# Kernel tuning notes

Hardware: AMD Instinct MI355X
Metric: run time of the kernel (lower is better)

## Reference

```python
import jax, jax.numpy as jnp
import numpy as np

N_NODES = 50000
N_EDGES = 800000
D_IN = 256
D_OUT = 96


def setup_inputs() -> dict:
    key = jax.random.key(0)
    k1, k2, k3 = jax.random.split(key, 3)
    x = jax.random.normal(k1, (N_NODES, D_IN), dtype=jnp.float32)
    edge_index = jax.random.randint(k2, (2, N_EDGES), 0, N_NODES, dtype=jnp.int64)
    # Glorot-like init for the GCN weight, zeros bias (bias_init=zeros_)
    W = jax.random.normal(k3, (D_IN, D_OUT), dtype=jnp.float32) * (1.0 / np.sqrt(D_IN))
    b = jnp.zeros((D_OUT,), dtype=jnp.float32)
    return {"x": x, "edge_index": edge_index, "W": W, "b": b}


def reference(x, edge_index, W, b):
    # GCNConv with normalize=False, add_self_loops=False:
    #   h = x @ W                      [N, D_OUT]
    #   out[dst] = sum over edges of h[src]
    #   out += bias (added after aggregation)
    src, dst = edge_index[0], edge_index[1]
    h = x @ W                                  # dense projection [N, D_OUT]
    msgs = h[src]                              # gather [E, D_OUT]
    out = jax.ops.segment_sum(msgs, dst, num_segments=x.shape[0])  # scatter-add
    return out + b
```

## Files before the change

### kernel.cpp

```cpp
#include <hip/hip_runtime.h>
#include <hip/hip_bf16.h>

#define N_NODES 50000
#define N_EDGES 800000
#define D_IN 256
#define D_OUT 96

#define NB 196
#define CAP 5120
#define KA_EPT 16
#define KA_BLOCKS ((N_EDGES + 256 * KA_EPT - 1) / (256 * KA_EPT))

typedef short bf16x8 __attribute__((ext_vector_type(8)));
typedef float f32x4 __attribute__((ext_vector_type(4)));

static __device__ inline ushort f2bf(float f) {
    union { __hip_bfloat16 h; ushort s; } u;
    u.h = __float2bfloat16(f);
    return u.s;
}
static __device__ inline float bfhi2f(unsigned int hibits) {
    union { unsigned int u; float f; } v; v.u = hibits; return v.f;
}

__global__ __launch_bounds__(256) void gcn_wt_kernel(
    const float* __restrict__ W, ushort* __restrict__ wT) {
    int c = blockIdx.x;
    int k = threadIdx.x;
    wT[c * D_IN + k] = f2bf(W[k * D_OUT + c]);
}

#define WLDS_K 264

__global__ __launch_bounds__(256) void gcn_gemm_mfma(
    const float* __restrict__ x, const ushort* __restrict__ wT,
    ushort* __restrict__ hB) {
    __shared__ ushort Wlds[96 * WLDS_K];

    const int tid = threadIdx.x;
#pragma unroll
    for (int it = 0; it < 12; ++it) {
        int i   = tid + it * 256;
        int c   = i >> 5;
        int k8  = (i & 31) << 3;
        uint4 v = reinterpret_cast<const uint4*>(wT)[i];
        *reinterpret_cast<uint4*>(&Wlds[c * WLDS_K + k8]) = v;
    }
    __syncthreads();

    const int lane = tid & 63;
    const int wave = tid >> 6;
    const int l15  = lane & 15;
    const int lk   = (lane >> 4) * 8;
    const int arow = blockIdx.x * 64 + wave * 16 + l15;
    const bool aok = arow < N_NODES;
    const float* xrow = &x[(size_t)(aok ? arow : 0) * D_IN];

    f32x4 acc[6];
#pragma unroll
    for (int c = 0; c < 6; ++c) acc[c] = (f32x4){0.f, 0.f, 0.f, 0.f};

#pragma unroll
    for (int kc = 0; kc < D_IN; kc += 32) {
        float4 v0 = make_float4(0.f, 0.f, 0.f, 0.f);
        float4 v1 = make_float4(0.f, 0.f, 0.f, 0.f);
        if (aok) {
            v0 = *reinterpret_cast<const float4*>(&xrow[kc + lk]);
            v1 = *reinterpret_cast<const float4*>(&xrow[kc + lk + 4]);
        }
        bf16x8 a;
        a[0] = (short)f2bf(v0.x); a[1] = (short)f2bf(v0.y);
        a[2] = (short)f2bf(v0.z); a[3] = (short)f2bf(v0.w);
        a[4] = (short)f2bf(v1.x); a[5] = (short)f2bf(v1.y);
        a[6] = (short)f2bf(v1.z); a[7] = (short)f2bf(v1.w);
#pragma unroll
        for (int c = 0; c < 6; ++c) {
            bf16x8 bf = *reinterpret_cast<const bf16x8*>(
                &Wlds[(c * 16 + l15) * WLDS_K + kc + lk]);
            acc[c] = __builtin_amdgcn_mfma_f32_16x16x32_bf16(a, bf, acc[c], 0, 0, 0);
        }
    }

    const int rbase = blockIdx.x * 64 + wave * 16 + (lane >> 4) * 4;
#pragma unroll
    for (int r = 0; r < 4; ++r) {
        int orow = rbase + r;
        if (orow < N_NODES) {
#pragma unroll
            for (int c = 0; c < 6; ++c)
                hB[orow * D_OUT + c * 16 + l15] = f2bf(acc[c][r]);
        }
    }
}

__global__ __launch_bounds__(256) void gcn_partition_kernel(
    const int* __restrict__ ei, int* __restrict__ bucket_cursor,
    unsigned int* __restrict__ recs) {
    __shared__ int lhist[NB];
    __shared__ int lbase[NB];
    const int tid = threadIdx.x;
    if (tid < NB) lhist[tid] = 0;
    __syncthreads();

    const int e0 = blockIdx.x * (256 * KA_EPT) + tid;
    int bk[KA_EPT];
    int rk[KA_EPT];
    unsigned int rec[KA_EPT];
#pragma unroll
    for (int i = 0; i < KA_EPT; ++i) {
        int e = e0 + i * 256;
        bk[i] = -1;
        if (e < N_EDGES) {
            int src = ei[e];
            int dst = ei[N_EDGES + e];
            if ((unsigned)src < (unsigned)N_NODES && (unsigned)dst < (unsigned)N_NODES) {
                bk[i]  = dst >> 8;
                rec[i] = (unsigned)src | ((unsigned)(dst & 255) << 16);
                rk[i]  = atomicAdd(&lhist[bk[i]], 1);
            }
        }
    }
    __syncthreads();
    if (tid < NB) lbase[tid] = atomicAdd(&bucket_cursor[tid], lhist[tid]);
    __syncthreads();
#pragma unroll
    for (int i = 0; i < KA_EPT; ++i) {
        if (bk[i] >= 0) {
            int pos = lbase[bk[i]] + rk[i];
            if (pos < CAP)
                recs[bk[i] * CAP + pos] = rec[i];
        }
    }
}

__global__ __launch_bounds__(256) void gcn_bucket_csr_kernel(
    const unsigned int* __restrict__ recs, const int* __restrict__ bucket_cursor,
    ushort* __restrict__ sorted16, int* __restrict__ cnt, int* __restrict__ offs) {
    __shared__ int    hist[256];
    __shared__ int    scanb[256];
    __shared__ int    cur[256];
    __shared__ ushort loc[CAP];
    const int b = blockIdx.x;
    const int t = threadIdx.x;
    int size = bucket_cursor[b];
    if (size > CAP) size = CAP;

    hist[t] = 0;
    __syncthreads();
    for (int i = t; i < size; i += 256)
        atomicAdd(&hist[(recs[b * CAP + i] >> 16) & 255], 1);
    __syncthreads();

    int v = hist[t];
    scanb[t] = v;
    __syncthreads();
    for (int off = 1; off < 256; off <<= 1) {
        int u = (t >= off) ? scanb[t - off] : 0;
        __syncthreads();
        scanb[t] += u;
        __syncthreads();
    }
    int excl = scanb[t] - v;
    cur[t] = excl;
    __syncthreads();

    for (int i = t; i < size; i += 256) {
        unsigned int r = recs[b * CAP + i];
        int l = (r >> 16) & 255;
        int p = atomicAdd(&cur[l], 1);
        loc[p] = (ushort)(r & 0xffffu);
    }
    __syncthreads();

    for (int i = t; i < size; i += 256)
        sorted16[b * CAP + i] = loc[i];

    int node = b * 256 + t;
    if (node < N_NODES) {
        cnt[node]  = hist[t];
        offs[node] = b * CAP + excl;
    }
}

#define AGG_NPB 32

__global__ __launch_bounds__(384) void gcn_aggregate_kernel(
    const ushort* __restrict__ hB, const int* __restrict__ offs,
    const int* __restrict__ cnt, const ushort* __restrict__ sorted16,
    const float* __restrict__ b, float* __restrict__ out) {
    int t    = threadIdx.x;
    int nloc = t / 12;
    int d8   = t - nloc * 12;
    int node = blockIdx.x * AGG_NPB + nloc;
    if (node >= N_NODES) return;

    int start = offs[node];
    int deg   = cnt[node];

    float a[8];
#pragma unroll
    for (int j = 0; j < 8; ++j) a[j] = 0.f;

#define ACC8(v)                                           \
    a[0] += bfhi2f((v).x << 16);                          \
    a[1] += bfhi2f((v).x & 0xffff0000u);                  \
    a[2] += bfhi2f((v).y << 16);                          \
    a[3] += bfhi2f((v).y & 0xffff0000u);                  \
    a[4] += bfhi2f((v).z << 16);                          \
    a[5] += bfhi2f((v).z & 0xffff0000u);                  \
    a[6] += bfhi2f((v).w << 16);                          \
    a[7] += bfhi2f((v).w & 0xffff0000u);

    int i = 0;
    for (; i + 4 <= deg; i += 4) {
        int s0 = sorted16[start + i + 0];
        int s1 = sorted16[start + i + 1];
        int s2 = sorted16[start + i + 2];
        int s3 = sorted16[start + i + 3];
        uint4 v0 = *reinterpret_cast<const uint4*>(&hB[s0 * D_OUT + d8 * 8]);
        uint4 v1 = *reinterpret_cast<const uint4*>(&hB[s1 * D_OUT + d8 * 8]);
        uint4 v2 = *reinterpret_cast<const uint4*>(&hB[s2 * D_OUT + d8 * 8]);
        uint4 v3 = *reinterpret_cast<const uint4*>(&hB[s3 * D_OUT + d8 * 8]);
        ACC8(v0); ACC8(v1); ACC8(v2); ACC8(v3);
    }
    for (; i < deg; ++i) {
        int s = sorted16[start + i];
        uint4 v = *reinterpret_cast<const uint4*>(&hB[s * D_OUT + d8 * 8]);
        ACC8(v);
    }
#undef ACC8

    const float4* bp = reinterpret_cast<const float4*>(&b[d8 * 8]);
    float4 b0 = bp[0], b1 = bp[1];
    float4 o0 = make_float4(a[0] + b0.x, a[1] + b0.y, a[2] + b0.z, a[3] + b0.w);
    float4 o1 = make_float4(a[4] + b1.x, a[5] + b1.y, a[6] + b1.z, a[7] + b1.w);
    float4* op = reinterpret_cast<float4*>(&out[node * D_OUT + d8 * 8]);
    op[0] = o0;
    op[1] = o1;
}

extern "C" void kernel_launch(void* const* d_in, const int* in_sizes, int n_in,
                              void* d_out, int out_size, void* d_ws, size_t ws_size,
                              hipStream_t stream) {
    const float* x  = (const float*)d_in[0];
    const int*   ei = (const int*)d_in[1];
    const float* W  = (const float*)d_in[2];
    const float* b  = (const float*)d_in[3];
    float* out = (float*)d_out;

    char* ws = (char*)d_ws;
    ushort* hB            = (ushort*)(ws);
    ushort* wT            = (ushort*)(ws + 9600000);
    int*    cnt           = (int*)   (ws + 9649152);
    int*    offs          = (int*)   (ws + 9849152);
    int*    bucket_cursor = (int*)   (ws + 10049152);
    unsigned int* recs    = (unsigned int*)(ws + 10050176);
    ushort* sorted16      = (ushort*)(ws + 14064256);

    gcn_wt_kernel<<<dim3(96), 256, 0, stream>>>(W, wT);
    gcn_gemm_mfma<<<dim3((N_NODES + 63) / 64), 256, 0, stream>>>(x, wT, hB);

    hipMemsetAsync(bucket_cursor, 0, NB * sizeof(int), stream);
    gcn_partition_kernel<<<dim3(KA_BLOCKS), 256, 0, stream>>>(ei, bucket_cursor, recs);
    gcn_bucket_csr_kernel<<<dim3(NB), 256, 0, stream>>>(recs, bucket_cursor, sorted16, cnt, offs);

    gcn_aggregate_kernel<<<dim3((N_NODES + AGG_NPB - 1) / AGG_NPB), 384, 0, stream>>>(
        hB, offs, cnt, sorted16, b, out);
}
```

Measured before the change: 154.8 us.

## Fuse bucket CSR build with aggregation and fold cursor memset into weight kernel

Merges the per-bucket counting-sort kernel and the aggregation kernel into one kernel that sorts the source indices in LDS and then gathers straight from that LDS list. This removes the global sorted-index, count and offset arrays and one launch. Buckets shrink to 128 nodes (391 buckets, capacity 2560), and the hipMemsetAsync is replaced by zeroing the cursors inside the weight-transpose kernel. Each thread now accumulates 24 features instead of 8, which raises register pressure. Only 391 blocks run the aggregation, so there may be less parallelism to hide gather latency.

```diff
diff --git a/kernel.cpp b/kernel.cpp
--- a/kernel.cpp
+++ b/kernel.cpp
@@ -6,10 +6,12 @@
 #define D_IN 256
 #define D_OUT 96
 
-#define NB 196
-#define CAP 5120
-#define KA_EPT 16
-#define KA_BLOCKS ((N_EDGES + 256 * KA_EPT - 1) / (256 * KA_EPT))
+#define NBLK 391
+#define NTHR 512
+#define CAP  2560
+#define EPB  ((N_EDGES + NBLK - 1) / NBLK)
+#define EPT  ((EPB + NTHR - 1) / NTHR)
+#define WLDS_K 264
 
 typedef short bf16x8 __attribute__((ext_vector_type(8)));
 typedef float f32x4 __attribute__((ext_vector_type(4)));
@@ -24,13 +26,14 @@
 }
 
 __global__ __launch_bounds__(256) void gcn_wt_kernel(
-    const float* __restrict__ W, ushort* __restrict__ wT) {
+    const float* __restrict__ W, ushort* __restrict__ wT,
+    int* __restrict__ bucket_cursor) {
     int c = blockIdx.x;
     int k = threadIdx.x;
     wT[c * D_IN + k] = f2bf(W[k * D_OUT + c]);
-}
-
-#define WLDS_K 264
+    int gid = c * 256 + k;
+    if (gid < NBLK) bucket_cursor[gid] = 0;
+}
 
 __global__ __launch_bounds__(256) void gcn_gemm_mfma(
     const float* __restrict__ x, const ushort* __restrict__ wT,
@@ -93,38 +96,39 @@
     }
 }
 
-__global__ __launch_bounds__(256) void gcn_partition_kernel(
+__global__ __launch_bounds__(NTHR) void gcn_partition_kernel(
     const int* __restrict__ ei, int* __restrict__ bucket_cursor,
     unsigned int* __restrict__ recs) {
-    __shared__ int lhist[NB];
-    __shared__ int lbase[NB];
-    const int tid = threadIdx.x;
-    if (tid < NB) lhist[tid] = 0;
-    __syncthreads();
-
-    const int e0 = blockIdx.x * (256 * KA_EPT) + tid;
-    int bk[KA_EPT];
-    int rk[KA_EPT];
-    unsigned int rec[KA_EPT];
-#pragma unroll
-    for (int i = 0; i < KA_EPT; ++i) {
-        int e = e0 + i * 256;
+    __shared__ int lhist[NBLK];
+    __shared__ int lbase[NBLK];
+    const int t = threadIdx.x;
+    for (int i = t; i < NBLK; i += NTHR) lhist[i] = 0;
+    __syncthreads();
+
+    const int ebase = blockIdx.x * EPB;
+    const int eend  = min(ebase + EPB, N_EDGES);
+    int bk[EPT]; int rk[EPT]; unsigned int rec[EPT];
+#pragma unroll
+    for (int i = 0; i < EPT; ++i) {
+        int e = ebase + i * NTHR + t;
         bk[i] = -1;
-        if (e < N_EDGES) {
+        if (e < eend) {
             int src = ei[e];
             int dst = ei[N_EDGES + e];
-            if ((unsigned)src < (unsigned)N_NODES && (unsigned)dst < (unsigned)N_NODES) {
-                bk[i]  = dst >> 8;
-                rec[i] = (unsigned)src | ((unsigned)(dst & 255) << 16);
+            if ((unsigned)src < (unsigned)N_NODES &&
+                (unsigned)dst < (unsigned)N_NODES) {
+                bk[i]  = dst >> 7;
+                rec[i] = (unsigned)src | ((unsigned)(dst & 127) << 16);
                 rk[i]  = atomicAdd(&lhist[bk[i]], 1);
             }
         }
     }
     __syncthreads();
-    if (tid < NB) lbase[tid] = atomicAdd(&bucket_cursor[tid], lhist[tid]);
-    __syncthreads();
-#pragma unroll
-    for (int i = 0; i < KA_EPT; ++i) {
+    for (int i = t; i < NBLK; i += NTHR)
+        lbase[i] = atomicAdd(&bucket_cursor[i], lhist[i]);
+    __syncthreads();
+#pragma unroll
+    for (int i = 0; i < EPT; ++i) {
         if (bk[i] >= 0) {
             int pos = lbase[bk[i]] + rk[i];
             if (pos < CAP)
@@ -133,110 +137,115 @@
     }
 }
 
-__global__ __launch_bounds__(256) void gcn_bucket_csr_kernel(
-    const unsigned int* __restrict__ recs, const int* __restrict__ bucket_cursor,
-    ushort* __restrict__ sorted16, int* __restrict__ cnt, int* __restrict__ offs) {
-    __shared__ int    hist[256];
-    __shared__ int    scanb[256];
-    __shared__ int    cur[256];
+__global__ __launch_bounds__(NTHR, 4) void gcn_csr_agg_kernel(
+    const ushort* __restrict__ hB, const int* __restrict__ bucket_cursor,
+    const unsigned int* __restrict__ recs, const float* __restrict__ bias,
+    float* __restrict__ out) {
+    __shared__ unsigned int srec[CAP];
     __shared__ ushort loc[CAP];
+    __shared__ int hist[128];
+    __shared__ int scanb[128];
+    __shared__ int cur[128];
     const int b = blockIdx.x;
     const int t = threadIdx.x;
     int size = bucket_cursor[b];
     if (size > CAP) size = CAP;
 
-    hist[t] = 0;
-    __syncthreads();
-    for (int i = t; i < size; i += 256)
-        atomicAdd(&hist[(recs[b * CAP + i] >> 16) & 255], 1);
-    __syncthreads();
-
-    int v = hist[t];
-    scanb[t] = v;
-    __syncthreads();
-    for (int off = 1; off < 256; off <<= 1) {
-        int u = (t >= off) ? scanb[t - off] : 0;
+    if (t < 128) hist[t] = 0;
+    __syncthreads();
+    for (int i = t; i < size; i += NTHR) {
+        unsigned int r = recs[b * CAP + i];
+        srec[i] = r;
+        atomicAdd(&hist[(r >> 16) & 127], 1);
+    }
+    __syncthreads();
+    if (t < 128) scanb[t] = hist[t];
+    __syncthreads();
+    for (int off = 1; off < 128; off <<= 1) {
+        int u = 0;
+        if (t < 128 && t >= off) u = scanb[t - off];
         __syncthreads();
-        scanb[t] += u;
+        if (t < 128) scanb[t] += u;
         __syncthreads();
     }
-    int excl = scanb[t] - v;
-    cur[t] = excl;
-    __syncthreads();
-
-    for (int i = t; i < size; i += 256) {
-        unsigned int r = recs[b * CAP + i];
-        int l = (r >> 16) & 255;
+    if (t < 128) cur[t] = scanb[t] - hist[t];
+    __syncthreads();
+    for (int i = t; i < size; i += NTHR) {
+        unsigned int r = srec[i];
+        int l = (r >> 16) & 127;
         int p = atomicAdd(&cur[l], 1);
         loc[p] = (ushort)(r & 0xffffu);
     }
     __syncthreads();
 
-    for (int i = t; i < size; i += 256)
-        sorted16[b * CAP + i] = loc[i];
-
-    int node = b * 256 + t;
-    if (node < N_NODES) {
-        cnt[node]  = hist[t];
-        offs[node] = b * CAP + excl;
-    }
-}
-
-#define AGG_NPB 32
-
-__global__ __launch_bounds__(384) void gcn_aggregate_kernel(
-    const ushort* __restrict__ hB, const int* __restrict__ offs,
-    const int* __restrict__ cnt, const ushort* __restrict__ sorted16,
-    const float* __restrict__ b, float* __restrict__ out) {
-    int t    = threadIdx.x;
-    int nloc = t / 12;
-    int d8   = t - nloc * 12;
-    int node = blockIdx.x * AGG_NPB + nloc;
+    const int nl   = t >> 2;
+    const int fs   = t & 3;
+    const int node = b * 128 + nl;
     if (node >= N_NODES) return;
 
-    int start = offs[node];
-    int deg   = cnt[node];
-
-    float a[8];
-#pragma unroll
-    for (int j = 0; j < 8; ++j) a[j] = 0.f;
-
-#define ACC8(v)                                           \
-    a[0] += bfhi2f((v).x << 16);                          \
-    a[1] += bfhi2f((v).x & 0xffff0000u);                  \
-    a[2] += bfhi2f((v).y << 16);                          \
-    a[3] += bfhi2f((v).y & 0xffff0000u);                  \
-    a[4] += bfhi2f((v).z << 16);                          \
-    a[5] += bfhi2f((v).z & 0xffff0000u);                  \
-    a[6] += bfhi2f((v).w << 16);                          \
-    a[7] += bfhi2f((v).w & 0xffff0000u);
+    int deg   = hist[nl];
+    int start = cur[nl] - deg;
+
+    float a[24];
+#pragma unroll
+    for (int j = 0; j < 24; ++j) a[j] = 0.f;
+
+#define ACC8V(v, B)                                \
+    a[B+0] += bfhi2f((v).x << 16);                 \
+    a[B+1] += bfhi2f((v).x & 0xffff0000u);         \
+    a[B+2] += bfhi2f((v).y << 16);                 \
+    a[B+3] += bfhi2f((v).y & 0xffff0000u);         \
+    a[B+4] += bfhi2f((v).z << 16);                 \
+    a[B+5] += bfhi2f((v).z & 0xffff0000u);         \
+    a[B+6] += bfhi2f((v).w << 16);                 \
+    a[B+7] += bfhi2f((v).w & 0xffff0000u);
 
     int i = 0;
     for (; i + 4 <= deg; i += 4) {
-        int s0 = sorted16[start + i + 0];
-        int s1 = sorted16[start + i + 1];
-        int s2 = sorted16[start + i + 2];
-        int s3 = sorted16[start + i + 3];
-        uint4 v0 = *reinterpret_cast<const uint4*>(&hB[s0 * D_OUT + d8 * 8]);
-        uint4 v1 = *reinterpret_cast<const uint4*>(&hB[s1 * D_OUT + d8 * 8]);
-        uint4 v2 = *reinterpret_cast<const uint4*>(&hB[s2 * D_OUT + d8 * 8]);
-        uint4 v3 = *reinterpret_cast<const uint4*>(&hB[s3 * D_OUT + d8 * 8]);
-        ACC8(v0); ACC8(v1); ACC8(v2); ACC8(v3);
+        int s0 = loc[start + i + 0];
+        int s1 = loc[start + i + 1];
+        int s2 = loc[start + i + 2];
+        int s3 = loc[start + i + 3];
+        const ushort* h0 = &hB[s0 * D_OUT + fs * 24];
+        const ushort* h1 = &hB[s1 * D_OUT + fs * 24];
+        const ushort* h2 = &hB[s2 * D_OUT + fs * 24];
+        const ushort* h3 = &hB[s3 * D_OUT + fs * 24];
+        uint4 v00 = *reinterpret_cast<const uint4*>(h0 + 0);
+        uint4 v01 = *reinterpret_cast<const uint4*>(h0 + 8);
+        uint4 v02 = *reinterpret_cast<const uint4*>(h0 + 16);
+        uint4 v10 = *reinterpret_cast<const uint4*>(h1 + 0);
+        uint4 v11 = *reinterpret_cast<const uint4*>(h1 + 8);
+        uint4 v12 = *reinterpret_cast<const uint4*>(h1 + 16);
+        uint4 v20 = *reinterpret_cast<const uint4*>(h2 + 0);
+        uint4 v21 = *reinterpret_cast<const uint4*>(h2 + 8);
+        uint4 v22 = *reinterpret_cast<const uint4*>(h2 + 16);
+        uint4 v30 = *reinterpret_cast<const uint4*>(h3 + 0);
+        uint4 v31 = *reinterpret_cast<const uint4*>(h3 + 8);
+        uint4 v32 = *reinterpret_cast<const uint4*>(h3 + 16);
+        ACC8V(v00, 0); ACC8V(v01, 8); ACC8V(v02, 16);
+        ACC8V(v10, 0); ACC8V(v11, 8); ACC8V(v12, 16);
+        ACC8V(v20, 0); ACC8V(v21, 8); ACC8V(v22, 16);
+        ACC8V(v30, 0); ACC8V(v31, 8); ACC8V(v32, 16);
     }
     for (; i < deg; ++i) {
-        int s = sorted16[start + i];
-        uint4 v = *reinterpret_cast<const uint4*>(&hB[s * D_OUT + d8 * 8]);
-        ACC8(v);
-    }
-#undef ACC8
-
-    const float4* bp = reinterpret_cast<const float4*>(&b[d8 * 8]);
-    float4 b0 = bp[0], b1 = bp[1];
-    float4 o0 = make_float4(a[0] + b0.x, a[1] + b0.y, a[2] + b0.z, a[3] + b0.w);
-    float4 o1 = make_float4(a[4] + b1.x, a[5] + b1.y, a[6] + b1.z, a[7] + b1.w);
-    float4* op = reinterpret_cast<float4*>(&out[node * D_OUT + d8 * 8]);
-    op[0] = o0;
-    op[1] = o1;
+        int s = loc[start + i];
+        const ushort* hp = &hB[s * D_OUT + fs * 24];
+        uint4 v0 = *reinterpret_cast<const uint4*>(hp + 0);
+        uint4 v1 = *reinterpret_cast<const uint4*>(hp + 8);
+        uint4 v2 = *reinterpret_cast<const uint4*>(hp + 16);
+        ACC8V(v0, 0); ACC8V(v1, 8); ACC8V(v2, 16);
+    }
+#undef ACC8V
+
+    const float4* bp = reinterpret_cast<const float4*>(&bias[fs * 24]);
+    float* op = &out[node * D_OUT + fs * 24];
+#pragma unroll
+    for (int j = 0; j < 6; ++j) {
+        float4 bv = bp[j];
+        float4 o  = make_float4(a[j*4+0] + bv.x, a[j*4+1] + bv.y,
+                                a[j*4+2] + bv.z, a[j*4+3] + bv.w);
+        *reinterpret_cast<float4*>(op + j * 4) = o;
+    }
 }
 
 extern "C" void kernel_launch(void* const* d_in, const int* in_sizes, int n_in,
@@ -249,21 +258,15 @@
     float* out = (float*)d_out;
 
     char* ws = (char*)d_ws;
-    ushort* hB            = (ushort*)(ws);
-    ushort* wT            = (ushort*)(ws + 9600000);
-    int*    cnt           = (int*)   (ws + 9649152);
-    int*    offs          = (int*)   (ws + 9849152);
-    int*    bucket_cursor = (int*)   (ws + 10049152);
-    unsigned int* recs    = (unsigned int*)(ws + 10050176);
-    ushort* sorted16      = (ushort*)(ws + 14064256);
-
-    gcn_wt_kernel<<<dim3(96), 256, 0, stream>>>(W, wT);
+    ushort*       hB     = (ushort*)(ws);
+    ushort*       wT     = (ushort*)(ws + 9600000);
+    int*          cursor = (int*)   (ws + 9649152);
+    unsigned int* recs   = (unsigned int*)(ws + 9651200);
+
+    gcn_wt_kernel<<<dim3(96), 256, 0, stream>>>(W, wT, cursor);
     gcn_gemm_mfma<<<dim3((N_NODES + 63) / 64), 256, 0, stream>>>(x, wT, hB);
 
-    hipMemsetAsync(bucket_cursor, 0, NB * sizeof(int), stream);
-    gcn_partition_kernel<<<dim3(KA_BLOCKS), 256, 0, stream>>>(ei, bucket_cursor, recs);
-    gcn_bucket_csr_kernel<<<dim3(NB), 256, 0, stream>>>(recs, bucket_cursor, sorted16, cnt, offs);
-
-    gcn_aggregate_kernel<<<dim3((N_NODES + AGG_NPB - 1) / AGG_NPB), 384, 0, stream>>>(
-        hB, offs, cnt, sorted16, b, out);
-}
+    gcn_partition_kernel<<<dim3(NBLK), NTHR, 0, stream>>>(ei, cursor, recs);
+
+    gcn_csr_agg_kernel<<<dim3(NBLK), NTHR, 0, stream>>>(hB, cursor, recs, b, out);
+}
```

After: 145.8 us. 5.9% less time.
